# Optimization experiments

Measured on AMD Instinct MI355X. Metric: run time of the kernel, lower is better.

The kernel has to match this reference:

```python
import jax, jax.numpy as jnp
import numpy as np
import math

EMBED_DIM = 512
NUM_HEADS = 8
HEAD_DIM = EMBED_DIM // NUM_HEADS


def setup_inputs() -> dict:
    key = jax.random.key(0)
    ks = jax.random.split(key, 11)
    s = 1.0 / math.sqrt(EMBED_DIM)
    x = jax.random.normal(ks[0], (8, EMBED_DIM, 32, 32), dtype=jnp.float32)
    Wq = jax.random.uniform(ks[1], (EMBED_DIM, EMBED_DIM), jnp.float32, -s, s)
    bq = jax.random.uniform(ks[2], (EMBED_DIM,), jnp.float32, -s, s)
    Wk = jax.random.uniform(ks[3], (EMBED_DIM, EMBED_DIM), jnp.float32, -s, s)
    bk = jax.random.uniform(ks[4], (EMBED_DIM,), jnp.float32, -s, s)
    Wv = jax.random.uniform(ks[5], (EMBED_DIM, EMBED_DIM), jnp.float32, -s, s)
    bv = jax.random.uniform(ks[6], (EMBED_DIM,), jnp.float32, -s, s)
    Wo = jax.random.uniform(ks[7], (EMBED_DIM, EMBED_DIM), jnp.float32, -s, s)
    bo = jax.random.uniform(ks[8], (EMBED_DIM,), jnp.float32, -s, s)
    gamma = jnp.ones((EMBED_DIM,), jnp.float32)
    beta = jnp.zeros((EMBED_DIM,), jnp.float32)
    return {"x": x, "Wq": Wq, "bq": bq, "Wk": Wk, "bk": bk, "Wv": Wv,
            "bv": bv, "Wo": Wo, "bo": bo, "gamma": gamma, "beta": beta}


def layer_norm(x, gamma, beta, eps=1e-5):
    mu = jnp.mean(x, axis=-1, keepdims=True)
    var = jnp.mean(jnp.square(x - mu), axis=-1, keepdims=True)
    return (x - mu) * jax.lax.rsqrt(var + eps) * gamma + beta


def reference(x, Wq, bq, Wk, bk, Wv, bv, Wo, bo, gamma, beta):
    B, C, H, W = x.shape
    S = H * W
    # [B, S, C]
    x_flat = x.reshape(B, C, S).transpose(0, 2, 1)
    residual = x_flat
    xn = layer_norm(x_flat, gamma, beta)
    # torch Linear: y = x @ W^T + b
    q = (xn @ Wq.T + bq).reshape(B, S, NUM_HEADS, HEAD_DIM)
    k = (xn @ Wk.T + bk).reshape(B, S, NUM_HEADS, HEAD_DIM)
    v = (xn @ Wv.T + bv).reshape(B, S, NUM_HEADS, HEAD_DIM)
    scale = 1.0 / math.sqrt(HEAD_DIM)
    scores = jnp.einsum('bqhd,bkhd->bhqk', q, k) * scale
    attn = jax.nn.softmax(scores, axis=-1)  # dropout is identity in eval
    out = jnp.einsum('bhqk,bkhd->bqhd', attn, v).reshape(B, S, C)
    out = out @ Wo.T + bo + residual
    return out.transpose(0, 2, 1).reshape(B, C, H, W)
```

## Files before the change

### kernel.cpp

```cpp
#include <hip/hip_runtime.h>
#include <hip/hip_bf16.h>

typedef __bf16 bf16_t;
typedef __bf16 bf16x8 __attribute__((ext_vector_type(8)));
typedef float floatx4 __attribute__((ext_vector_type(4)));

#define EMBED 512
#define S_LEN 1024
#define NH 8
#define HD 64
#define LDK 1056
#define LDV 1088

#define MFMA16(a, b, c) __builtin_amdgcn_mfma_f32_16x16x32_bf16(a, b, c, 0, 0, 0)

static __device__ __forceinline__ bf16_t f2bf(float f) {
    unsigned int x = __builtin_bit_cast(unsigned int, f);
    unsigned int lsb = (x >> 16) & 1u;
    x += 0x7fffu + lsb;
    unsigned short u = (unsigned short)(x >> 16);
    return __builtin_bit_cast(bf16_t, u);
}
static __device__ __forceinline__ float bf2f(bf16_t v) {
    unsigned short u = __builtin_bit_cast(unsigned short, v);
    unsigned int x = ((unsigned int)u) << 16;
    return __builtin_bit_cast(float, x);
}
static __device__ __forceinline__ unsigned int pack2(float lo, float hi) {
    return (__builtin_bit_cast(unsigned int, lo) >> 16) |
           (__builtin_bit_cast(unsigned int, hi) & 0xFFFF0000u);
}

__global__ __launch_bounds__(256) void cvt4_kernel(const float* __restrict__ s0,
                                                   const float* __restrict__ s1,
                                                   const float* __restrict__ s2,
                                                   const float* __restrict__ s3,
                                                   bf16_t* __restrict__ d0,
                                                   bf16_t* __restrict__ d1,
                                                   bf16_t* __restrict__ d2,
                                                   bf16_t* __restrict__ d3) {
    const float* s; bf16_t* d;
    switch (blockIdx.y) {
        case 0:  s = s0; d = d0; break;
        case 1:  s = s1; d = d1; break;
        case 2:  s = s2; d = d2; break;
        default: s = s3; d = d3; break;
    }
    int i = (blockIdx.x * 256 + threadIdx.x) * 8;
#pragma unroll
    for (int j = 0; j < 8; ++j) d[i + j] = f2bf(s[i + j]);
}

__global__ __launch_bounds__(256) void ln_stats_kernel(const float* __restrict__ x,
                                                       float* __restrict__ muA,
                                                       float* __restrict__ rsA) {
    int bid = blockIdx.x;
    int b = bid >> 5, s0 = (bid & 31) * 32;
    int t = threadIdx.x, tc = t >> 5, ts = t & 31;
    const float* xp = x + (size_t)b * EMBED * S_LEN + s0 + ts;
    float sm = 0.f, sq = 0.f;
    for (int i = 0; i < 64; ++i) {
        float v = xp[(size_t)(tc * 64 + i) * S_LEN];
        sm += v; sq += v * v;
    }
    __shared__ float Sm[8][32], Sq[8][32];
    Sm[tc][ts] = sm; Sq[tc][ts] = sq;
    __syncthreads();
    if (t < 32) {
        float m = 0.f, q = 0.f;
#pragma unroll
        for (int j = 0; j < 8; ++j) { m += Sm[j][t]; q += Sq[j][t]; }
        float mu = m * (1.0f / EMBED);
        float var = q * (1.0f / EMBED) - mu * mu;
        muA[b * S_LEN + s0 + t] = mu;
        rsA[b * S_LEN + s0 + t] = rsqrtf(var + 1e-5f);
    }
}

__global__ __launch_bounds__(256) void ln_tr_kernel(const float* __restrict__ x,
                                                    const float* __restrict__ muA,
                                                    const float* __restrict__ rsA,
                                                    const float* __restrict__ gamma,
                                                    const float* __restrict__ beta,
                                                    bf16_t* __restrict__ xn) {
    __shared__ float T[32][33];
    int tx = threadIdx.x & 31, ty = threadIdx.x >> 5;
    int b = blockIdx.z, c0 = blockIdx.y * 32, s0 = blockIdx.x * 32;
#pragma unroll
    for (int i = 0; i < 4; ++i) {
        int cr = ty + i * 8;
        T[cr][tx] = x[((size_t)b * EMBED + c0 + cr) * S_LEN + s0 + tx];
    }
    __syncthreads();
    float g = gamma[c0 + tx], be = beta[c0 + tx];
#pragma unroll
    for (int i = 0; i < 4; ++i) {
        int sr = ty + i * 8;
        float mu = muA[b * S_LEN + s0 + sr];
        float rs = rsA[b * S_LEN + s0 + sr];
        xn[((size_t)b * S_LEN + s0 + sr) * EMBED + c0 + tx] =
            f2bf((T[tx][sr] - mu) * rs * g + be);
    }
}

__global__ __launch_bounds__(256) void gemm_kernel(const bf16_t* __restrict__ X,
                                                   const bf16_t* __restrict__ W,
                                                   const float* __restrict__ b0,
                                                   const float* __restrict__ b1,
                                                   bf16_t* __restrict__ Y, int ldY) {
    __shared__ __align__(16) bf16_t Wl[2][128 * 72];
    int t = threadIdx.x;
    int col0 = blockIdx.y * 128, row0 = blockIdx.x * 128;
    int scol = t >> 1, sseg = (t & 1) * 32;
    const bf16_t* wsrc = W + (size_t)(col0 + scol) * EMBED + sseg;
    {
        bf16x8 r0 = *(const bf16x8*)(wsrc);
        bf16x8 r1 = *(const bf16x8*)(wsrc + 8);
        bf16x8 r2 = *(const bf16x8*)(wsrc + 16);
        bf16x8 r3 = *(const bf16x8*)(wsrc + 24);
        bf16_t* d = &Wl[0][scol * 72 + sseg];
        *(bf16x8*)d = r0;        *(bf16x8*)(d + 8) = r1;
        *(bf16x8*)(d + 16) = r2; *(bf16x8*)(d + 24) = r3;
    }
    int lane = t & 63, w = t >> 6, g = lane >> 4, n16 = lane & 15;
    int rw0 = row0 + w * 32;
    const bf16_t* xr0 = X + (size_t)(rw0 + n16) * EMBED + g * 8;
    const bf16_t* xr1 = xr0 + (size_t)16 * EMBED;
    bf16x8 a00 = *(const bf16x8*)(xr0);
    bf16x8 a01 = *(const bf16x8*)(xr0 + 32);
    bf16x8 a10 = *(const bf16x8*)(xr1);
    bf16x8 a11 = *(const bf16x8*)(xr1 + 32);
    __syncthreads();
    floatx4 acc[2][8] = {};
#pragma unroll
    for (int kc = 0; kc < 8; ++kc) {
        bf16x8 p0, p1, p2, p3, na00, na01, na10, na11;
        if (kc < 7) {
            int ko = (kc + 1) * 64;
            p0 = *(const bf16x8*)(wsrc + ko);
            p1 = *(const bf16x8*)(wsrc + ko + 8);
            p2 = *(const bf16x8*)(wsrc + ko + 16);
            p3 = *(const bf16x8*)(wsrc + ko + 24);
            na00 = *(const bf16x8*)(xr0 + ko);
            na01 = *(const bf16x8*)(xr0 + ko + 32);
            na10 = *(const bf16x8*)(xr1 + ko);
            na11 = *(const bf16x8*)(xr1 + ko + 32);
        }
        const bf16_t* wl = &Wl[kc & 1][0];
#pragma unroll
        for (int kk = 0; kk < 2; ++kk) {
            bf16x8 s0 = (kk == 0) ? a00 : a01;
            bf16x8 s1 = (kk == 0) ? a10 : a11;
#pragma unroll
            for (int nt = 0; nt < 8; ++nt) {
                bf16x8 bfr = *(const bf16x8*)(&wl[(nt * 16 + n16) * 72 + kk * 32 + g * 8]);
                acc[0][nt] = MFMA16(s0, bfr, acc[0][nt]);
                acc[1][nt] = MFMA16(s1, bfr, acc[1][nt]);
            }
        }
        if (kc < 7) {
            bf16_t* d = &Wl[(kc + 1) & 1][scol * 72 + sseg];
            *(bf16x8*)d = p0;        *(bf16x8*)(d + 8) = p1;
            *(bf16x8*)(d + 16) = p2; *(bf16x8*)(d + 24) = p3;
            a00 = na00; a01 = na01; a10 = na10; a11 = na11;
        }
        __syncthreads();
    }
#pragma unroll
    for (int ar = 0; ar < 2; ++ar)
#pragma unroll
        for (int nt = 0; nt < 8; ++nt) {
            int col = col0 + nt * 16 + n16;
            float bv = (col < 512) ? b0[col] : b1[col - 512];
#pragma unroll
            for (int r = 0; r < 4; ++r) {
                int row = rw0 + ar * 16 + g * 4 + r;
                Y[(size_t)row * ldY + col] = f2bf(acc[ar][nt][r] + bv);
            }
        }
}

__global__ __launch_bounds__(256) void wsgemm_vt_kernel(const bf16_t* __restrict__ Wb,
                                                        const bf16_t* __restrict__ act,
                                                        const float* __restrict__ bias,
                                                        bf16_t* __restrict__ vtb) {
    __shared__ __align__(16) bf16_t Al[2][64 * 72];
    int b = blockIdx.z, n0 = blockIdx.x * 64, m0 = blockIdx.y * 128;
    int t = threadIdx.x;
    int srow = t >> 2, sseg = (t & 3) * 16;
    const bf16_t* asrc = act + ((size_t)b * S_LEN + n0 + srow) * EMBED + sseg;
    {
        bf16x8 r0 = *(const bf16x8*)(asrc);
        bf16x8 r1 = *(const bf16x8*)(asrc + 8);
        bf16_t* d = &Al[0][srow * 72 + sseg];
        *(bf16x8*)d = r0; *(bf16x8*)(d + 8) = r1;
    }
    int lane = t & 63, w = t >> 6, g = lane >> 4, n16 = lane & 15;
    int mw = m0 + w * 32;
    const bf16_t* wr0 = Wb + (size_t)(mw + n16) * EMBED + g * 8;
    const bf16_t* wr1 = wr0 + (size_t)16 * EMBED;
    bf16x8 a00 = *(const bf16x8*)(wr0);
    bf16x8 a01 = *(const bf16x8*)(wr0 + 32);
    bf16x8 a10 = *(const bf16x8*)(wr1);
    bf16x8 a11 = *(const bf16x8*)(wr1 + 32);
    __syncthreads();
    floatx4 acc[2][4] = {};
#pragma unroll
    for (int kc = 0; kc < 8; ++kc) {
        bf16x8 p0, p1, na00, na01, na10, na11;
        if (kc < 7) {
            int ko = (kc + 1) * 64;
            p0 = *(const bf16x8*)(asrc + ko);
            p1 = *(const bf16x8*)(asrc + ko + 8);
            na00 = *(const bf16x8*)(wr0 + ko);
            na01 = *(const bf16x8*)(wr0 + ko + 32);
            na10 = *(const bf16x8*)(wr1 + ko);
            na11 = *(const bf16x8*)(wr1 + ko + 32);
        }
        const bf16_t* al = &Al[kc & 1][0];
#pragma unroll
        for (int kk = 0; kk < 2; ++kk) {
            bf16x8 s0 = (kk == 0) ? a00 : a01;
            bf16x8 s1 = (kk == 0) ? a10 : a11;
#pragma unroll
            for (int nt = 0; nt < 4; ++nt) {
                bf16x8 bfr = *(const bf16x8*)(&al[(nt * 16 + n16) * 72 + kk * 32 + g * 8]);
                acc[0][nt] = MFMA16(s0, bfr, acc[0][nt]);
                acc[1][nt] = MFMA16(s1, bfr, acc[1][nt]);
            }
        }
        if (kc < 7) {
            bf16_t* d = &Al[(kc + 1) & 1][srow * 72 + sseg];
            *(bf16x8*)d = p0; *(bf16x8*)(d + 8) = p1;
            a00 = na00; a01 = na01; a10 = na10; a11 = na11;
        }
        __syncthreads();
    }
#pragma unroll
    for (int ar = 0; ar < 2; ++ar)
#pragma unroll
        for (int r = 0; r < 4; ++r) {
            int row = mw + ar * 16 + g * 4 + r;
            float bv = bias[row];
#pragma unroll
            for (int nt = 0; nt < 4; ++nt) {
                int col = n0 + nt * 16 + n16;
                vtb[((size_t)b * EMBED + row) * LDV + col] = f2bf(acc[ar][nt][r] + bv);
            }
        }
}

__global__ __launch_bounds__(256) void wsgemm_out_kernel(const bf16_t* __restrict__ Wb,
                                                         const bf16_t* __restrict__ act,
                                                         const float* __restrict__ bias,
                                                         const float* __restrict__ xres,
                                                         float* __restrict__ out) {
    __shared__ __align__(16) bf16_t Al[2][64 * 72];
    int b = blockIdx.z, n0 = blockIdx.x * 64, m0 = blockIdx.y * 128;
    int t = threadIdx.x;
    int srow = t >> 2, sseg = (t & 3) * 16;
    const bf16_t* asrc = act + ((size_t)b * S_LEN + n0 + srow) * EMBED + sseg;
    {
        bf16x8 r0 = *(const bf16x8*)(asrc);
        bf16x8 r1 = *(const bf16x8*)(asrc + 8);
        bf16_t* d = &Al[0][srow * 72 + sseg];
        *(bf16x8*)d = r0; *(bf16x8*)(d + 8) = r1;
    }
    int lane = t & 63, w = t >> 6, g = lane >> 4, n16 = lane & 15;
    int mw = m0 + w * 32;
    const bf16_t* wr0 = Wb + (size_t)(mw + n16) * EMBED + g * 8;
    const bf16_t* wr1 = wr0 + (size_t)16 * EMBED;
    bf16x8 a00 = *(const bf16x8*)(wr0);
    bf16x8 a01 = *(const bf16x8*)(wr0 + 32);
    bf16x8 a10 = *(const bf16x8*)(wr1);
    bf16x8 a11 = *(const bf16x8*)(wr1 + 32);
    __syncthreads();
    floatx4 acc[2][4] = {};
#pragma unroll
    for (int kc = 0; kc < 8; ++kc) {
        bf16x8 p0, p1, na00, na01, na10, na11;
        if (kc < 7) {
            int ko = (kc + 1) * 64;
            p0 = *(const bf16x8*)(asrc + ko);
            p1 = *(const bf16x8*)(asrc + ko + 8);
            na00 = *(const bf16x8*)(wr0 + ko);
            na01 = *(const bf16x8*)(wr0 + ko + 32);
            na10 = *(const bf16x8*)(wr1 + ko);
            na11 = *(const bf16x8*)(wr1 + ko + 32);
        }
        const bf16_t* al = &Al[kc & 1][0];
#pragma unroll
        for (int kk = 0; kk < 2; ++kk) {
            bf16x8 s0 = (kk == 0) ? a00 : a01;
            bf16x8 s1 = (kk == 0) ? a10 : a11;
#pragma unroll
            for (int nt = 0; nt < 4; ++nt) {
                bf16x8 bfr = *(const bf16x8*)(&al[(nt * 16 + n16) * 72 + kk * 32 + g * 8]);
                acc[0][nt] = MFMA16(s0, bfr, acc[0][nt]);
                acc[1][nt] = MFMA16(s1, bfr, acc[1][nt]);
            }
        }
        if (kc < 7) {
            bf16_t* d = &Al[(kc + 1) & 1][srow * 72 + sseg];
            *(bf16x8*)d = p0; *(bf16x8*)(d + 8) = p1;
            a00 = na00; a01 = na01; a10 = na10; a11 = na11;
        }
        __syncthreads();
    }
#pragma unroll
    for (int ar = 0; ar < 2; ++ar)
#pragma unroll
        for (int r = 0; r < 4; ++r) {
            int row = mw + ar * 16 + g * 4 + r;
            float bv = bias[row];
#pragma unroll
            for (int nt = 0; nt < 4; ++nt) {
                int col = n0 + nt * 16 + n16;
                size_t oi = ((size_t)b * EMBED + row) * S_LEN + col;
                out[oi] = acc[ar][nt][r] + bv + xres[oi];
            }
        }
}

__global__ __launch_bounds__(256) void attn_kernel(const bf16_t* __restrict__ qk,
                                                   const bf16_t* __restrict__ vt,
                                                   bf16_t* __restrict__ o) {
    __shared__ __align__(16) bf16_t Kt[2][64 * 72];
    __shared__ __align__(16) bf16_t Vl2[2][64 * 72];
    __shared__ __align__(16) unsigned int Pl[4][2][16 * 36];
    int bid = blockIdx.x;
    int bh = bid & 63, qt = bid >> 6;
    int b = bh >> 3, h = bh & 7;
    int t = threadIdx.x, w = t >> 6, lane = t & 63, g = lane >> 4, n16 = lane & 15;
    size_t baseQK = (size_t)b * S_LEN * LDK;
    size_t baseV  = ((size_t)b * EMBED + h * HD) * LDV;
    int qA = qt * 128 + w * 32 + n16;

    const bf16_t* qpA = qk + baseQK + (size_t)qA * LDK + h * HD + g * 8;
    const bf16_t* qpB = qpA + (size_t)16 * LDK;
    bf16x8 qa0 = *(const bf16x8*)(qpA);
    bf16x8 qa1 = *(const bf16x8*)(qpA + 32);
    bf16x8 qb0 = *(const bf16x8*)(qpB);
    bf16x8 qb1 = *(const bf16x8*)(qpB + 32);
#pragma unroll
    for (int j = 0; j < 8; ++j) {
        qa0[j] = f2bf(bf2f(qa0[j]) * 0.125f);
        qa1[j] = f2bf(bf2f(qa1[j]) * 0.125f);
        qb0[j] = f2bf(bf2f(qb0[j]) * 0.125f);
        qb1[j] = f2bf(bf2f(qb1[j]) * 0.125f);
    }
    const bf16_t* kbase = qk + baseQK + 512 + h * HD;
    const bf16_t* vbase = vt + baseV;

    int srow = t >> 2, scol = (t & 3) * 16;
    const bf16_t* ksrc = kbase + (size_t)srow * LDK + scol;
    const bf16_t* vsrc = vbase + (size_t)srow * LDV + scol;
    {
        bf16x8 k0 = *(const bf16x8*)(ksrc);
        bf16x8 k1 = *(const bf16x8*)(ksrc + 8);
        bf16x8 v0 = *(const bf16x8*)(vsrc);
        bf16x8 v1 = *(const bf16x8*)(vsrc + 8);
        bf16_t* kd = &Kt[0][srow * 72 + scol];
        bf16_t* vd = &Vl2[0][srow * 72 + scol];
        *(bf16x8*)kd = k0; *(bf16x8*)(kd + 8) = k1;
        *(bf16x8*)vd = v0; *(bf16x8*)(vd + 8) = v1;
    }

    float lsA[4] = {}, lsB[4] = {};
    floatx4 oaccA[4] = {}, oaccB[4] = {};
    unsigned int* PLa = &Pl[w][0][0];
    unsigned int* PLb = &Pl[w][1][0];

    for (int it = 0; it < 16; ++it) {
        int cur = it & 1, nxt = cur ^ 1;
        __syncthreads();
        bf16x8 pk0, pk1, pv0, pv1;
        if (it < 15) {
            const bf16_t* kp = ksrc + (size_t)(it + 1) * 64 * LDK;
            pk0 = *(const bf16x8*)(kp);
            pk1 = *(const bf16x8*)(kp + 8);
            const bf16_t* vp = vsrc + (it + 1) * 64;
            pv0 = *(const bf16x8*)(vp);
            pv1 = *(const bf16x8*)(vp + 8);
        }
        const bf16_t* Kl = &Kt[cur][0];
        const bf16_t* Vl = &Vl2[cur][0];
        floatx4 sA[4], sB[4];
#pragma unroll
        for (int kb = 0; kb < 4; ++kb) {
            bf16x8 k0 = *(const bf16x8*)(&Kl[(kb * 16 + n16) * 72 + g * 8]);
            bf16x8 k1 = *(const bf16x8*)(&Kl[(kb * 16 + n16) * 72 + 32 + g * 8]);
            sA[kb] = floatx4{-12.f, -12.f, -12.f, -12.f};
            sA[kb] = MFMA16(k0, qa0, sA[kb]);
            sA[kb] = MFMA16(k1, qa1, sA[kb]);
            sB[kb] = floatx4{-12.f, -12.f, -12.f, -12.f};
            sB[kb] = MFMA16(k0, qb0, sB[kb]);
            sB[kb] = MFMA16(k1, qb1, sB[kb]);
        }
        if (it < 15) {
            bf16_t* kd = &Kt[nxt][srow * 72 + scol];
            bf16_t* vd = &Vl2[nxt][srow * 72 + scol];
            *(bf16x8*)kd = pk0; *(bf16x8*)(kd + 8) = pk1;
            *(bf16x8*)vd = pv0; *(bf16x8*)(vd + 8) = pv1;
        }
#pragma unroll
        for (int kb = 0; kb < 4; ++kb)
#pragma unroll
            for (int r = 0; r < 4; ++r) {
                float eA = __expf(fminf(sA[kb][r], 40.f));
                sA[kb][r] = eA; lsA[kb] += eA;
                float eB = __expf(fminf(sB[kb][r], 40.f));
                sB[kb][r] = eB; lsB[kb] += eB;
            }
#pragma unroll
        for (int kb = 0; kb < 4; ++kb) {
            uint2 prA, prB;
            prA.x = pack2(sA[kb][0], sA[kb][1]);
            prA.y = pack2(sA[kb][2], sA[kb][3]);
            *(uint2*)&PLa[n16 * 36 + kb * 8 + g * 2] = prA;
            prB.x = pack2(sB[kb][0], sB[kb][1]);
            prB.y = pack2(sB[kb][2], sB[kb][3]);
            *(uint2*)&PLb[n16 * 36 + kb * 8 + g * 2] = prB;
        }
        uint4 uA0 = *(const uint4*)&PLa[n16 * 36 + g * 4];
        uint4 uA1 = *(const uint4*)&PLa[n16 * 36 + 16 + g * 4];
        uint4 uB0 = *(const uint4*)&PLb[n16 * 36 + g * 4];
        uint4 uB1 = *(const uint4*)&PLb[n16 * 36 + 16 + g * 4];
        bf16x8 pfA0 = __builtin_bit_cast(bf16x8, uA0);
        bf16x8 pfA1 = __builtin_bit_cast(bf16x8, uA1);
        bf16x8 pfB0 = __builtin_bit_cast(bf16x8, uB0);
        bf16x8 pfB1 = __builtin_bit_cast(bf16x8, uB1);
#pragma unroll
        for (int dt = 0; dt < 4; ++dt) {
            bf16x8 v0 = *(const bf16x8*)(&Vl[(dt * 16 + n16) * 72 + g * 8]);
            bf16x8 v1 = *(const bf16x8*)(&Vl[(dt * 16 + n16) * 72 + 32 + g * 8]);
            oaccA[dt] = MFMA16(v0, pfA0, oaccA[dt]);
            oaccA[dt] = MFMA16(v1, pfA1, oaccA[dt]);
            oaccB[dt] = MFMA16(v0, pfB0, oaccB[dt]);
            oaccB[dt] = MFMA16(v1, pfB1, oaccB[dt]);
        }
    }
    float lA = (lsA[0] + lsA[1]) + (lsA[2] + lsA[3]);
    lA += __shfl_xor(lA, 16);
    lA += __shfl_xor(lA, 32);
    float lB = (lsB[0] + lsB[1]) + (lsB[2] + lsB[3]);
    lB += __shfl_xor(lB, 16);
    lB += __shfl_xor(lB, 32);
    float rlA = 1.0f / lA, rlB = 1.0f / lB;
    size_t orowA = ((size_t)b * S_LEN + qA) * EMBED + h * HD;
    size_t orowB = orowA + (size_t)16 * EMBED;
#pragma unroll
    for (int dt = 0; dt < 4; ++dt) {
        uint2 prA, prB;
        prA.x = pack2(oaccA[dt][0] * rlA, oaccA[dt][1] * rlA);
        prA.y = pack2(oaccA[dt][2] * rlA, oaccA[dt][3] * rlA);
        *(uint2*)(o + orowA + dt * 16 + g * 4) = prA;
        prB.x = pack2(oaccB[dt][0] * rlB, oaccB[dt][1] * rlB);
        prB.y = pack2(oaccB[dt][2] * rlB, oaccB[dt][3] * rlB);
        *(uint2*)(o + orowB + dt * 16 + g * 4) = prB;
    }
}

extern "C" void kernel_launch(void* const* d_in, const int* in_sizes, int n_in,
                              void* d_out, int out_size, void* d_ws, size_t ws_size,
                              hipStream_t stream) {
    const float* x     = (const float*)d_in[0];
    const float* Wq    = (const float*)d_in[1];
    const float* bq    = (const float*)d_in[2];
    const float* Wk    = (const float*)d_in[3];
    const float* bk    = (const float*)d_in[4];
    const float* Wv    = (const float*)d_in[5];
    const float* bv    = (const float*)d_in[6];
    const float* Wo    = (const float*)d_in[7];
    const float* bo    = (const float*)d_in[8];
    const float* gamma = (const float*)d_in[9];
    const float* beta  = (const float*)d_in[10];
    float* out = (float*)d_out;

    char* ws = (char*)d_ws;
    bf16_t* xn   = (bf16_t*)ws;
    bf16_t* qkb  = (bf16_t*)(ws + 8388608);
    bf16_t* wqk  = (bf16_t*)(ws + 25690112);
    bf16_t* wv   = (bf16_t*)(ws + 26738688);
    bf16_t* wo   = (bf16_t*)(ws + 27262976);
    float*  muA  = (float*)(ws + 27787264);
    float*  rsA  = (float*)(ws + 27820032);
    bf16_t* ab   = xn;

    bf16_t* vtb = (bf16_t*)d_out;

    cvt4_kernel<<<dim3(128, 4), 256, 0, stream>>>(Wq, Wk, Wv, Wo,
                                                  wqk, wqk + 262144, wv, wo);
    ln_stats_kernel<<<dim3(256), 256, 0, stream>>>(x, muA, rsA);
    ln_tr_kernel<<<dim3(32, 16, 8), 256, 0, stream>>>(x, muA, rsA, gamma, beta, xn);
    gemm_kernel<<<dim3(64, 8), 256, 0, stream>>>(xn, wqk, bq, bk, qkb, LDK);
    wsgemm_vt_kernel<<<dim3(16, 4, 8), 256, 0, stream>>>(wv, xn, bv, vtb);
    attn_kernel<<<dim3(512), 256, 0, stream>>>(qkb, vtb, ab);
    wsgemm_out_kernel<<<dim3(16, 4, 8), 256, 0, stream>>>(wo, ab, bo, x, out);
}
```

Measured before the change: 174.8 us.

## Fuse V projection into QK GEMM and transpose V inside attention

Removes the separate weight-stationary V-transpose GEMM and computes Q, K and V in a single GEMM launch writing a combined row-major buffer with stride 1568. The attention kernel now loads V in row-major order and transposes it into shared memory with scalar element stores. This saves one kernel launch and improves GEMM occupancy through a larger grid, but the scalar transposed LDS writes may cause bank conflicts and add instructions in the attention inner loop.

```diff
diff --git a/kernel.cpp b/kernel.cpp
--- a/kernel.cpp
+++ b/kernel.cpp
@@ -9,8 +9,7 @@
 #define S_LEN 1024
 #define NH 8
 #define HD 64
-#define LDK 1056
-#define LDV 1088
+#define LDQ 1568
 
 #define MFMA16(a, b, c) __builtin_amdgcn_mfma_f32_16x16x32_bf16(a, b, c, 0, 0, 0)
 
@@ -107,6 +106,7 @@
                                                    const bf16_t* __restrict__ W,
                                                    const float* __restrict__ b0,
                                                    const float* __restrict__ b1,
+                                                   const float* __restrict__ b2,
                                                    bf16_t* __restrict__ Y, int ldY) {
     __shared__ __align__(16) bf16_t Wl[2][128 * 72];
     int t = threadIdx.x;
@@ -171,81 +171,12 @@
 #pragma unroll
         for (int nt = 0; nt < 8; ++nt) {
             int col = col0 + nt * 16 + n16;
-            float bv = (col < 512) ? b0[col] : b1[col - 512];
+            float bv = (col < 512) ? b0[col]
+                     : (col < 1024) ? b1[col - 512] : b2[col - 1024];
 #pragma unroll
             for (int r = 0; r < 4; ++r) {
                 int row = rw0 + ar * 16 + g * 4 + r;
                 Y[(size_t)row * ldY + col] = f2bf(acc[ar][nt][r] + bv);
-            }
-        }
-}
-
-__global__ __launch_bounds__(256) void wsgemm_vt_kernel(const bf16_t* __restrict__ Wb,
-                                                        const bf16_t* __restrict__ act,
-                                                        const float* __restrict__ bias,
-                                                        bf16_t* __restrict__ vtb) {
-    __shared__ __align__(16) bf16_t Al[2][64 * 72];
-    int b = blockIdx.z, n0 = blockIdx.x * 64, m0 = blockIdx.y * 128;
-    int t = threadIdx.x;
-    int srow = t >> 2, sseg = (t & 3) * 16;
-    const bf16_t* asrc = act + ((size_t)b * S_LEN + n0 + srow) * EMBED + sseg;
-    {
-        bf16x8 r0 = *(const bf16x8*)(asrc);
-        bf16x8 r1 = *(const bf16x8*)(asrc + 8);
-        bf16_t* d = &Al[0][srow * 72 + sseg];
-        *(bf16x8*)d = r0; *(bf16x8*)(d + 8) = r1;
-    }
-    int lane = t & 63, w = t >> 6, g = lane >> 4, n16 = lane & 15;
-    int mw = m0 + w * 32;
-    const bf16_t* wr0 = Wb + (size_t)(mw + n16) * EMBED + g * 8;
-    const bf16_t* wr1 = wr0 + (size_t)16 * EMBED;
-    bf16x8 a00 = *(const bf16x8*)(wr0);
-    bf16x8 a01 = *(const bf16x8*)(wr0 + 32);
-    bf16x8 a10 = *(const bf16x8*)(wr1);
-    bf16x8 a11 = *(const bf16x8*)(wr1 + 32);
-    __syncthreads();
-    floatx4 acc[2][4] = {};
-#pragma unroll
-    for (int kc = 0; kc < 8; ++kc) {
-        bf16x8 p0, p1, na00, na01, na10, na11;
-        if (kc < 7) {
-            int ko = (kc + 1) * 64;
-            p0 = *(const bf16x8*)(asrc + ko);
-            p1 = *(const bf16x8*)(asrc + ko + 8);
-            na00 = *(const bf16x8*)(wr0 + ko);
-            na01 = *(const bf16x8*)(wr0 + ko + 32);
-            na10 = *(const bf16x8*)(wr1 + ko);
-            na11 = *(const bf16x8*)(wr1 + ko + 32);
-        }
-        const bf16_t* al = &Al[kc & 1][0];
-#pragma unroll
-        for (int kk = 0; kk < 2; ++kk) {
-            bf16x8 s0 = (kk == 0) ? a00 : a01;
-            bf16x8 s1 = (kk == 0) ? a10 : a11;
-#pragma unroll
-            for (int nt = 0; nt < 4; ++nt) {
-                bf16x8 bfr = *(const bf16x8*)(&al[(nt * 16 + n16) * 72 + kk * 32 + g * 8]);
-                acc[0][nt] = MFMA16(s0, bfr, acc[0][nt]);
-                acc[1][nt] = MFMA16(s1, bfr, acc[1][nt]);
-            }
-        }
-        if (kc < 7) {
-            bf16_t* d = &Al[(kc + 1) & 1][srow * 72 + sseg];
-            *(bf16x8*)d = p0; *(bf16x8*)(d + 8) = p1;
-            a00 = na00; a01 = na01; a10 = na10; a11 = na11;
-        }
-        __syncthreads();
-    }
-#pragma unroll
-    for (int ar = 0; ar < 2; ++ar)
-#pragma unroll
-        for (int r = 0; r < 4; ++r) {
-            int row = mw + ar * 16 + g * 4 + r;
-            float bv = bias[row];
-#pragma unroll
-            for (int nt = 0; nt < 4; ++nt) {
-                int col = n0 + nt * 16 + n16;
-                vtb[((size_t)b * EMBED + row) * LDV + col] = f2bf(acc[ar][nt][r] + bv);
             }
         }
 }
@@ -322,22 +253,20 @@
         }
 }
 
-__global__ __launch_bounds__(256) void attn_kernel(const bf16_t* __restrict__ qk,
-                                                   const bf16_t* __restrict__ vt,
+__global__ __launch_bounds__(256) void attn_kernel(const bf16_t* __restrict__ qkv,
                                                    bf16_t* __restrict__ o) {
     __shared__ __align__(16) bf16_t Kt[2][64 * 72];
-    __shared__ __align__(16) bf16_t Vl2[2][64 * 72];
+    __shared__ __align__(16) bf16_t Vt[2][64 * 72];
     __shared__ __align__(16) unsigned int Pl[4][2][16 * 36];
     int bid = blockIdx.x;
     int bh = bid & 63, qt = bid >> 6;
     int b = bh >> 3, h = bh & 7;
     int t = threadIdx.x, w = t >> 6, lane = t & 63, g = lane >> 4, n16 = lane & 15;
-    size_t baseQK = (size_t)b * S_LEN * LDK;
-    size_t baseV  = ((size_t)b * EMBED + h * HD) * LDV;
+    size_t baseQ = (size_t)b * S_LEN * LDQ + h * HD;
     int qA = qt * 128 + w * 32 + n16;
 
-    const bf16_t* qpA = qk + baseQK + (size_t)qA * LDK + h * HD + g * 8;
-    const bf16_t* qpB = qpA + (size_t)16 * LDK;
+    const bf16_t* qpA = qkv + baseQ + (size_t)qA * LDQ + g * 8;
+    const bf16_t* qpB = qpA + (size_t)16 * LDQ;
     bf16x8 qa0 = *(const bf16x8*)(qpA);
     bf16x8 qa1 = *(const bf16x8*)(qpA + 32);
     bf16x8 qb0 = *(const bf16x8*)(qpB);
@@ -349,21 +278,22 @@
         qb0[j] = f2bf(bf2f(qb0[j]) * 0.125f);
         qb1[j] = f2bf(bf2f(qb1[j]) * 0.125f);
     }
-    const bf16_t* kbase = qk + baseQK + 512 + h * HD;
-    const bf16_t* vbase = vt + baseV;
 
     int srow = t >> 2, scol = (t & 3) * 16;
-    const bf16_t* ksrc = kbase + (size_t)srow * LDK + scol;
-    const bf16_t* vsrc = vbase + (size_t)srow * LDV + scol;
+    const bf16_t* ksrc = qkv + baseQ + 512 + (size_t)srow * LDQ + scol;
+    const bf16_t* vsrc = qkv + baseQ + 1024 + (size_t)srow * LDQ + scol;
     {
         bf16x8 k0 = *(const bf16x8*)(ksrc);
         bf16x8 k1 = *(const bf16x8*)(ksrc + 8);
         bf16x8 v0 = *(const bf16x8*)(vsrc);
         bf16x8 v1 = *(const bf16x8*)(vsrc + 8);
         bf16_t* kd = &Kt[0][srow * 72 + scol];
-        bf16_t* vd = &Vl2[0][srow * 72 + scol];
         *(bf16x8*)kd = k0; *(bf16x8*)(kd + 8) = k1;
-        *(bf16x8*)vd = v0; *(bf16x8*)(vd + 8) = v1;
+#pragma unroll
+        for (int j = 0; j < 8; ++j) {
+            Vt[0][(scol + j) * 72 + srow]     = v0[j];
+            Vt[0][(scol + 8 + j) * 72 + srow] = v1[j];
+        }
     }
 
     float lsA[4] = {}, lsB[4] = {};
@@ -376,15 +306,14 @@
         __syncthreads();
         bf16x8 pk0, pk1, pv0, pv1;
         if (it < 15) {
-            const bf16_t* kp = ksrc + (size_t)(it + 1) * 64 * LDK;
-            pk0 = *(const bf16x8*)(kp);
-            pk1 = *(const bf16x8*)(kp + 8);
-            const bf16_t* vp = vsrc + (it + 1) * 64;
-            pv0 = *(const bf16x8*)(vp);
-            pv1 = *(const bf16x8*)(vp + 8);
+            size_t adv = (size_t)(it + 1) * 64 * LDQ;
+            pk0 = *(const bf16x8*)(ksrc + adv);
+            pk1 = *(const bf16x8*)(ksrc + adv + 8);
+            pv0 = *(const bf16x8*)(vsrc + adv);
+            pv1 = *(const bf16x8*)(vsrc + adv + 8);
         }
         const bf16_t* Kl = &Kt[cur][0];
-        const bf16_t* Vl = &Vl2[cur][0];
+        const bf16_t* Vl = &Vt[cur][0];
         floatx4 sA[4], sB[4];
 #pragma unroll
         for (int kb = 0; kb < 4; ++kb) {
@@ -399,9 +328,12 @@
         }
         if (it < 15) {
             bf16_t* kd = &Kt[nxt][srow * 72 + scol];
-            bf16_t* vd = &Vl2[nxt][srow * 72 + scol];
             *(bf16x8*)kd = pk0; *(bf16x8*)(kd + 8) = pk1;
-            *(bf16x8*)vd = pv0; *(bf16x8*)(vd + 8) = pv1;
+#pragma unroll
+            for (int j = 0; j < 8; ++j) {
+                Vt[nxt][(scol + j) * 72 + srow]     = pv0[j];
+                Vt[nxt][(scol + 8 + j) * 72 + srow] = pv1[j];
+            }
         }
 #pragma unroll
         for (int kb = 0; kb < 4; ++kb)
@@ -478,23 +410,20 @@
     float* out = (float*)d_out;
 
     char* ws = (char*)d_ws;
-    bf16_t* xn   = (bf16_t*)ws;
-    bf16_t* qkb  = (bf16_t*)(ws + 8388608);
-    bf16_t* wqk  = (bf16_t*)(ws + 25690112);
-    bf16_t* wv   = (bf16_t*)(ws + 26738688);
-    bf16_t* wo   = (bf16_t*)(ws + 27262976);
-    float*  muA  = (float*)(ws + 27787264);
-    float*  rsA  = (float*)(ws + 27820032);
-    bf16_t* ab   = xn;
-
-    bf16_t* vtb = (bf16_t*)d_out;
+    bf16_t* xn    = (bf16_t*)ws;
+    bf16_t* qkvb  = (bf16_t*)(ws + 8388608);
+    bf16_t* wqkv  = (bf16_t*)(ws + 34078720);
+    bf16_t* wo    = (bf16_t*)(ws + 35651584);
+    float*  muA   = (float*)(ws + 36175872);
+    float*  rsA   = (float*)(ws + 36208640);
+    bf16_t* ab    = xn;
 
     cvt4_kernel<<<dim3(128, 4), 256, 0, stream>>>(Wq, Wk, Wv, Wo,
-                                                  wqk, wqk + 262144, wv, wo);
+                                                  wqkv, wqkv + 262144,
+                                                  wqkv + 524288, wo);
     ln_stats_kernel<<<dim3(256), 256, 0, stream>>>(x, muA, rsA);
     ln_tr_kernel<<<dim3(32, 16, 8), 256, 0, stream>>>(x, muA, rsA, gamma, beta, xn);
-    gemm_kernel<<<dim3(64, 8), 256, 0, stream>>>(xn, wqk, bq, bk, qkb, LDK);
-    wsgemm_vt_kernel<<<dim3(16, 4, 8), 256, 0, stream>>>(wv, xn, bv, vtb);
-    attn_kernel<<<dim3(512), 256, 0, stream>>>(qkb, vtb, ab);
+    gemm_kernel<<<dim3(64, 12), 256, 0, stream>>>(xn, wqkv, bq, bk, bv, qkvb, LDQ);
+    attn_kernel<<<dim3(512), 256, 0, stream>>>(qkvb, ab);
     wsgemm_out_kernel<<<dim3(16, 4, 8), 256, 0, stream>>>(wo, ab, bo, x, out);
 }
```

New measurement: 180.1 us. +3.0%, slower.
